# Kernel tuning notes

Measured on AMD Instinct MI355X. Metric: run time of the kernel, lower is better.

## Reference

```python
import jax, jax.numpy as jnp
import numpy as np

B, L, N, D = 4096, 50, 50, 128
STD = 0.1


def setup_inputs() -> dict:
    key = jax.random.key(0)
    ks = jax.random.split(key, 6)
    seq_idx = jax.random.randint(ks[0], (B, L), 0, N, dtype=jnp.int32)
    mask = jnp.ones((B, L), dtype=jnp.int32)
    node_vectors = jax.random.normal(ks[1], (B, N, D), dtype=jnp.float32)
    u = lambda k, shp: jax.random.uniform(k, shp, jnp.float32, -STD, STD)
    return {
        "sequence_of_indexes": seq_idx,
        "mask": mask,
        "node_vectors": node_vectors,
        "batch_size": B,
        "W_last": u(ks[2], (D, D)),      # dense_last_item kernel (no bias)
        "W_seq": u(ks[3], (D, D)),       # dense_sequence_items kernel
        "b_seq": jnp.zeros((D,), jnp.float32),  # dense_sequence_items bias
        "W_alpha": u(ks[4], (D, 1)),     # dense_alpha kernel (no bias)
    }


def reference(sequence_of_indexes, mask, node_vectors, batch_size,
              W_last, W_seq, b_seq, W_alpha):
    maskf = mask.astype(jnp.float32)                          # [B, L]
    seq_len = jnp.sum(maskf, axis=1).astype(jnp.int32)        # [B]
    rows = jnp.arange(batch_size)
    # last item index per session, then gather its node vector
    last_idx = sequence_of_indexes[rows, seq_len - 1]         # [B]
    v_n = node_vectors[rows, last_idx]                        # [B, D]
    # per-batch embedding lookup: node_vectors[b, seq_idx[b]]
    v_i = jnp.take_along_axis(node_vectors, sequence_of_indexes[..., None], axis=1)  # [B, L, D]
    vn_proj = (v_n @ W_last)[:, None, :]                      # [B, 1, D]
    vi_proj = v_i @ W_seq + b_seq                             # [B, L, D]
    alpha = jax.nn.sigmoid(vn_proj + vi_proj) @ W_alpha       # [B, L, 1]
    alpha = alpha * maskf[..., None]
    session_graph = jnp.sum(alpha * v_i, axis=1)              # [B, D]
    return v_n, session_graph
```

## Files before the change

kernel.cpp:

```cpp
#include <hip/hip_runtime.h>
#include <math.h>

#define BB 4096
#define LL 50
#define NN 50
#define DD 128
#define STR 136

typedef short bf16x8 __attribute__((ext_vector_type(8)));
typedef float f32x4  __attribute__((ext_vector_type(4)));

static __device__ inline unsigned short f32_to_bf16_rne(float f) {
    unsigned int u = __float_as_uint(f);
    u += 0x7FFFu + ((u >> 16) & 1u);
    return (unsigned short)(u >> 16);
}

__global__ void prep_w(const float* __restrict__ W_seq,
                       const float* __restrict__ W_last,
                       unsigned short* __restrict__ ws)
{
    int t = blockIdx.x * blockDim.x + threadIdx.x;
    int lane = t & 63;
    int nt   = (t >> 6) & 7;
    int kk   = t >> 9;
    const float* W = (kk < 4) ? W_seq : W_last;
    int kb = (kk & 3) * 32 + (lane >> 4) * 8;
    int n  = nt * 16 + (lane & 15);
    unsigned short* dst = ws + (size_t)t * 8;
    #pragma unroll
    for (int j = 0; j < 8; ++j)
        dst[j] = f32_to_bf16_rne(W[(kb + j) * DD + n]);
}

__global__ __launch_bounds__(256, 4) void sess_attn(
    const int*   __restrict__ seq_idx,
    const int*   __restrict__ mask,
    const float* __restrict__ nodes,
    const float* __restrict__ b_seq,
    const float* __restrict__ W_alpha,
    const unsigned short* __restrict__ wfrag,
    float*       __restrict__ out)
{
    const int b    = blockIdx.x;
    const int tid  = threadIdx.x;
    const int lane = tid & 63;
    const int wave = tid >> 6;
    const int col  = lane & 15;
    const int quad = lane >> 4;

    __shared__ __align__(16) float s_f[NN * DD];
    __shared__ __align__(16) unsigned short s_nbf[NN * STR];
    __shared__ float s_alpha[64];
    __shared__ float s_cnt[64];
    __shared__ int   s_last;

    const float* nb = nodes + (size_t)b * (NN * DD);

    int pm = 0, pi = 0;
    if (tid < 64) {
        pm = (tid < LL) ? mask[b * LL + tid]    : 0;
        pi = (tid < LL) ? seq_idx[b * LL + tid] : 0;
    }

    #pragma unroll
    for (int i = 0; i < 6; ++i) {
        int p  = i * 256 + tid;
        int r  = p >> 5;
        int Bk = p & 31;
        const float* src = nb + r * DD + ((Bk ^ (r & 7)) << 2);
        __builtin_amdgcn_global_load_lds(
            (const __attribute__((address_space(1))) unsigned int*)src,
            (__attribute__((address_space(3))) unsigned int*)(&s_f[(i * 256 + wave * 64) * 4]),
            16, 0, 0);
    }
    if (tid < 64) {
        int p  = 1536 + tid;
        int r  = p >> 5, Bk = p & 31;
        const float* src = nb + r * DD + ((Bk ^ (r & 7)) << 2);
        __builtin_amdgcn_global_load_lds(
            (const __attribute__((address_space(1))) unsigned int*)src,
            (__attribute__((address_space(3))) unsigned int*)(&s_f[1536 * 4]),
            16, 0, 0);
    }

    const bf16x8* wsf = (const bf16x8*)wfrag;
    bf16x8 bfS[8], bfL[8];
    #pragma unroll
    for (int kk = 0; kk < 4; ++kk)
        #pragma unroll
        for (int j2 = 0; j2 < 2; ++j2) {
            bfS[kk * 2 + j2] = wsf[(size_t)(((kk    ) * 8 + wave * 2 + j2) * 64 + lane)];
            bfL[kk * 2 + j2] = wsf[(size_t)(((kk + 4) * 8 + wave * 2 + j2) * 64 + lane)];
        }

    float bb_r[2], wa_r[2];
    #pragma unroll
    for (int j2 = 0; j2 < 2; ++j2) {
        int n = (wave * 2 + j2) * 16 + col;
        bb_r[j2] = b_seq[n];
        wa_r[j2] = W_alpha[n];
    }

    if (tid < 64) { s_alpha[tid] = 0.f; s_cnt[tid] = 0.f; }

    asm volatile("s_waitcnt vmcnt(0)" ::: "memory");
    #pragma unroll
    for (int i = 0; i < 6; ++i) {
        int p  = i * 256 + wave * 64 + lane;
        int r  = p >> 5, Bk = p & 31;
        float4 f = *(const float4*)&s_f[p * 4];
        ushort4 h;
        h.x = f32_to_bf16_rne(f.x);
        h.y = f32_to_bf16_rne(f.y);
        h.z = f32_to_bf16_rne(f.z);
        h.w = f32_to_bf16_rne(f.w);
        *(ushort4*)&s_nbf[r * STR + ((Bk ^ (r & 7)) << 2)] = h;
    }
    if (tid < 64) {
        int p  = 1536 + lane;
        int r  = p >> 5, Bk = p & 31;
        float4 f = *(const float4*)&s_f[p * 4];
        ushort4 h;
        h.x = f32_to_bf16_rne(f.x);
        h.y = f32_to_bf16_rne(f.y);
        h.z = f32_to_bf16_rne(f.z);
        h.w = f32_to_bf16_rne(f.w);
        *(ushort4*)&s_nbf[r * STR + ((Bk ^ (r & 7)) << 2)] = h;
    }

    if (tid < 64) {
        int mm = pm;
        mm += __shfl_xor(mm, 1);  mm += __shfl_xor(mm, 2);
        mm += __shfl_xor(mm, 4);  mm += __shfl_xor(mm, 8);
        mm += __shfl_xor(mm, 16); mm += __shfl_xor(mm, 32);
        int jl = mm - 1;
        if (jl < 0) jl += LL;
        int li = __shfl(pi, jl);
        if (tid == 0) s_last = li;
        if (tid < LL && pm) atomicAdd(&s_cnt[pi], (float)pm);
    }

    __syncthreads();

    const int last = s_last;
    const int sL   = last & 7;

    if (tid < DD)
        out[(size_t)b * DD + tid] =
            s_f[last * DD + (((tid >> 2) ^ sL) << 2) + (tid & 3)];

    f32x4 acc[4][2];
    #pragma unroll
    for (int m = 0; m < 4; ++m)
        #pragma unroll
        for (int j2 = 0; j2 < 2; ++j2)
            acc[m][j2] = (f32x4){0.f, 0.f, 0.f, 0.f};
    f32x4 accV[2];
    #pragma unroll
    for (int j2 = 0; j2 < 2; ++j2)
        accV[j2] = (f32x4){bb_r[j2], bb_r[j2], bb_r[j2], bb_r[j2]};

    #pragma unroll
    for (int kk = 0; kk < 4; ++kk) {
        const int co = kk * 32 + quad * 8;
        bf16x8 a[4];
        #pragma unroll
        for (int m = 0; m < 4; ++m) {
            int r = m * 16 + col;
            if (r > NN - 1) r = NN - 1;
            a[m] = *(const bf16x8*)&s_nbf[r * STR + co];
        }
        bf16x8 av = *(const bf16x8*)&s_nbf[last * STR + co];
        #pragma unroll
        for (int j2 = 0; j2 < 2; ++j2) {
            acc[0][j2] = __builtin_amdgcn_mfma_f32_16x16x32_bf16(a[0], bfS[kk * 2 + j2], acc[0][j2], 0, 0, 0);
            acc[1][j2] = __builtin_amdgcn_mfma_f32_16x16x32_bf16(a[1], bfS[kk * 2 + j2], acc[1][j2], 0, 0, 0);
            acc[2][j2] = __builtin_amdgcn_mfma_f32_16x16x32_bf16(a[2], bfS[kk * 2 + j2], acc[2][j2], 0, 0, 0);
            acc[3][j2] = __builtin_amdgcn_mfma_f32_16x16x32_bf16(a[3], bfS[kk * 2 + j2], acc[3][j2], 0, 0, 0);
            accV[j2]   = __builtin_amdgcn_mfma_f32_16x16x32_bf16(av,   bfL[kk * 2 + j2], accV[j2],   0, 0, 0);
        }
    }

    #pragma unroll
    for (int m = 0; m < 4; ++m) {
        float pr[4] = {0.f, 0.f, 0.f, 0.f};
        #pragma unroll
        for (int j2 = 0; j2 < 2; ++j2) {
            float waj = wa_r[j2];
            #pragma unroll
            for (int r = 0; r < 4; ++r) {
                float x = acc[m][j2][r] + accV[j2][r];
                float sig = 1.f / (1.f + __expf(-x));
                pr[r] = fmaf(sig, waj, pr[r]);
            }
        }
        #pragma unroll
        for (int r = 0; r < 4; ++r) {
            float vv = pr[r];
            vv += __shfl_xor(vv, 1);
            vv += __shfl_xor(vv, 2);
            vv += __shfl_xor(vv, 4);
            vv += __shfl_xor(vv, 8);
            int row = m * 16 + quad * 4 + r;
            if (col == 0 && row < NN) atomicAdd(&s_alpha[row], vv);
        }
    }
    __syncthreads();

    if (tid < DD) {
        const int Bd = tid >> 2, od = tid & 3;
        float acc2 = 0.f;
        #pragma unroll 10
        for (int n = 0; n < NN; ++n)
            acc2 = fmaf(s_cnt[n] * s_alpha[n],
                        s_f[n * DD + ((Bd ^ (n & 7)) << 2) + od], acc2);
        out[(size_t)BB * DD + (size_t)b * DD + tid] = acc2;
    }
}

extern "C" void kernel_launch(void* const* d_in, const int* in_sizes, int n_in,
                              void* d_out, int out_size, void* d_ws, size_t ws_size,
                              hipStream_t stream) {
    const int*   seq     = (const int*)  d_in[0];
    const int*   mask    = (const int*)  d_in[1];
    const float* nodes   = (const float*)d_in[2];
    const float* W_last  = (const float*)d_in[4];
    const float* W_seq   = (const float*)d_in[5];
    const float* b_seq   = (const float*)d_in[6];
    const float* W_alpha = (const float*)d_in[7];
    float*       out     = (float*)      d_out;

    unsigned short* wsf = (unsigned short*)d_ws;

    prep_w<<<16, 256, 0, stream>>>(W_seq, W_last, wsf);
    sess_attn<<<BB, 256, 0, stream>>>(seq, mask, nodes, b_seq, W_alpha, wsf, out);
}
```

Baseline: 179.2 us.

## Process eight sessions per block with double-buffered bf16 tiles and prefetch

Each block now handles eight consecutive batch entries. The next entry's node vectors are prefetched into LDS while the current one is multiplied, and the converted bf16 tile is double-buffered. Weight fragments and per-block setup are amortised over the eight entries, and the final weighted sum reads the bf16 tile instead of fp32. This reduces the grid to 512 blocks and lowers occupancy, risking poorer latency hiding, and slightly lowers the precision of the output sum.

```diff
diff --git a/kernel.cpp b/kernel.cpp
--- a/kernel.cpp
+++ b/kernel.cpp
@@ -6,14 +6,22 @@
 #define NN 50
 #define DD 128
 #define STR 136
+#define NB 8
+#define GRID 512
 
 typedef short bf16x8 __attribute__((ext_vector_type(8)));
 typedef float f32x4  __attribute__((ext_vector_type(4)));
+
+#define AS1 __attribute__((address_space(1)))
+#define AS3 __attribute__((address_space(3)))
 
 static __device__ inline unsigned short f32_to_bf16_rne(float f) {
     unsigned int u = __float_as_uint(f);
     u += 0x7FFFu + ((u >> 16) & 1u);
     return (unsigned short)(u >> 16);
+}
+static __device__ inline float bf16_to_f32(unsigned short h) {
+    return __uint_as_float(((unsigned int)h) << 16);
 }
 
 __global__ void prep_w(const float* __restrict__ W_seq,
@@ -33,7 +41,7 @@
         dst[j] = f32_to_bf16_rne(W[(kb + j) * DD + n]);
 }
 
-__global__ __launch_bounds__(256, 4) void sess_attn(
+__global__ __launch_bounds__(256, 2) void sess_attn(
     const int*   __restrict__ seq_idx,
     const int*   __restrict__ mask,
     const float* __restrict__ nodes,
@@ -42,46 +50,40 @@
     const unsigned short* __restrict__ wfrag,
     float*       __restrict__ out)
 {
-    const int b    = blockIdx.x;
+    const int blk  = blockIdx.x;
     const int tid  = threadIdx.x;
     const int lane = tid & 63;
     const int wave = tid >> 6;
     const int col  = lane & 15;
     const int quad = lane >> 4;
 
-    __shared__ __align__(16) float s_f[NN * DD];
-    __shared__ __align__(16) unsigned short s_nbf[NN * STR];
-    __shared__ float s_alpha[64];
-    __shared__ float s_cnt[64];
-    __shared__ int   s_last;
-
-    const float* nb = nodes + (size_t)b * (NN * DD);
-
-    int pm = 0, pi = 0;
-    if (tid < 64) {
-        pm = (tid < LL) ? mask[b * LL + tid]    : 0;
-        pi = (tid < LL) ? seq_idx[b * LL + tid] : 0;
-    }
-
-    #pragma unroll
-    for (int i = 0; i < 6; ++i) {
-        int p  = i * 256 + tid;
-        int r  = p >> 5;
-        int Bk = p & 31;
-        const float* src = nb + r * DD + ((Bk ^ (r & 7)) << 2);
-        __builtin_amdgcn_global_load_lds(
-            (const __attribute__((address_space(1))) unsigned int*)src,
-            (__attribute__((address_space(3))) unsigned int*)(&s_f[(i * 256 + wave * 64) * 4]),
-            16, 0, 0);
-    }
-    if (tid < 64) {
-        int p  = 1536 + tid;
-        int r  = p >> 5, Bk = p & 31;
-        const float* src = nb + r * DD + ((Bk ^ (r & 7)) << 2);
-        __builtin_amdgcn_global_load_lds(
-            (const __attribute__((address_space(1))) unsigned int*)src,
-            (__attribute__((address_space(3))) unsigned int*)(&s_f[1536 * 4]),
-            16, 0, 0);
+    __shared__ __align__(16) float          s_f[NN * DD];
+    __shared__ __align__(16) unsigned short s_nbf[2][NN * STR];
+    __shared__ float s_alpha[2][64];
+    __shared__ float s_cnt[NB][64];
+    __shared__ __align__(16) int s_mask[NB * LL];
+    __shared__ __align__(16) int s_sidx[NB * LL];
+    __shared__ int   s_last[NB];
+
+    const int b0 = blk * NB;
+
+    int4 m4, s4;
+    if (tid < 100) {
+        m4 = ((const int4*)(mask    + b0 * LL))[tid];
+        s4 = ((const int4*)(seq_idx + b0 * LL))[tid];
+    }
+
+    {
+        const float* nb = nodes + (size_t)b0 * (NN * DD);
+        #pragma unroll
+        for (int c = 0; c < 6; ++c)
+            __builtin_amdgcn_global_load_lds(
+                (const AS1 unsigned int*)(nb + (size_t)(c * 256 + tid) * 4),
+                (AS3 unsigned int*)(&s_f[(c * 256 + wave * 64) * 4]), 16, 0, 0);
+        if (tid < 64)
+            __builtin_amdgcn_global_load_lds(
+                (const AS1 unsigned int*)(nb + (size_t)(1536 + tid) * 4),
+                (AS3 unsigned int*)(&s_f[1536 * 4]), 16, 0, 0);
     }
 
     const bf16x8* wsf = (const bf16x8*)wfrag;
@@ -93,7 +95,6 @@
             bfS[kk * 2 + j2] = wsf[(size_t)(((kk    ) * 8 + wave * 2 + j2) * 64 + lane)];
             bfL[kk * 2 + j2] = wsf[(size_t)(((kk + 4) * 8 + wave * 2 + j2) * 64 + lane)];
         }
-
     float bb_r[2], wa_r[2];
     #pragma unroll
     for (int j2 = 0; j2 < 2; ++j2) {
@@ -102,34 +103,21 @@
         wa_r[j2] = W_alpha[n];
     }
 
-    if (tid < 64) { s_alpha[tid] = 0.f; s_cnt[tid] = 0.f; }
-
-    asm volatile("s_waitcnt vmcnt(0)" ::: "memory");
-    #pragma unroll
-    for (int i = 0; i < 6; ++i) {
-        int p  = i * 256 + wave * 64 + lane;
-        int r  = p >> 5, Bk = p & 31;
-        float4 f = *(const float4*)&s_f[p * 4];
-        ushort4 h;
-        h.x = f32_to_bf16_rne(f.x);
-        h.y = f32_to_bf16_rne(f.y);
-        h.z = f32_to_bf16_rne(f.z);
-        h.w = f32_to_bf16_rne(f.w);
-        *(ushort4*)&s_nbf[r * STR + ((Bk ^ (r & 7)) << 2)] = h;
-    }
-    if (tid < 64) {
-        int p  = 1536 + lane;
-        int r  = p >> 5, Bk = p & 31;
-        float4 f = *(const float4*)&s_f[p * 4];
-        ushort4 h;
-        h.x = f32_to_bf16_rne(f.x);
-        h.y = f32_to_bf16_rne(f.y);
-        h.z = f32_to_bf16_rne(f.z);
-        h.w = f32_to_bf16_rne(f.w);
-        *(ushort4*)&s_nbf[r * STR + ((Bk ^ (r & 7)) << 2)] = h;
-    }
-
-    if (tid < 64) {
+    #pragma unroll
+    for (int z = 0; z < 2; ++z) s_cnt[z * 4 + wave][lane] = 0.f;
+    if (tid < 64) { s_alpha[0][tid] = 0.f; s_alpha[1][tid] = 0.f; }
+    if (tid < 100) {
+        *(int4*)&s_mask[tid * 4] = m4;
+        *(int4*)&s_sidx[tid * 4] = s4;
+    }
+
+    __syncthreads();
+
+    #pragma unroll
+    for (int t2 = 0; t2 < 2; ++t2) {
+        int ib = wave * 2 + t2;
+        int pm = (lane < LL) ? s_mask[ib * LL + lane] : 0;
+        int pi = (lane < LL) ? s_sidx[ib * LL + lane] : 0;
         int mm = pm;
         mm += __shfl_xor(mm, 1);  mm += __shfl_xor(mm, 2);
         mm += __shfl_xor(mm, 4);  mm += __shfl_xor(mm, 8);
@@ -137,85 +125,130 @@
         int jl = mm - 1;
         if (jl < 0) jl += LL;
         int li = __shfl(pi, jl);
-        if (tid == 0) s_last = li;
-        if (tid < LL && pm) atomicAdd(&s_cnt[pi], (float)pm);
+        if (lane == 0) s_last[ib] = li;
+        if (lane < LL && pm) atomicAdd(&s_cnt[ib][pi], (float)pm);
     }
 
     __syncthreads();
 
-    const int last = s_last;
-    const int sL   = last & 7;
-
-    if (tid < DD)
-        out[(size_t)b * DD + tid] =
-            s_f[last * DD + (((tid >> 2) ^ sL) << 2) + (tid & 3)];
-
-    f32x4 acc[4][2];
-    #pragma unroll
-    for (int m = 0; m < 4; ++m)
+    const int r0 = col, r1 = 16 + col, r2 = 32 + col;
+    const int r3 = (48 + col > NN - 1) ? (NN - 1) : (48 + col);
+
+    for (int i = 0; i < NB; ++i) {
+        const int b   = b0 + i;
+        const int par = i & 1;
+
+        if (i >= 1 && tid < 64) s_alpha[(i - 1) & 1][tid] = 0.f;
+
+        #pragma unroll
+        for (int c = 0; c < 6; ++c) {
+            int p = c * 256 + tid;
+            int r = p >> 5, cc = (p & 31) * 4;
+            float4 f = *(const float4*)&s_f[p * 4];
+            ushort4 h;
+            h.x = f32_to_bf16_rne(f.x); h.y = f32_to_bf16_rne(f.y);
+            h.z = f32_to_bf16_rne(f.z); h.w = f32_to_bf16_rne(f.w);
+            *(ushort4*)&s_nbf[par][r * STR + cc] = h;
+        }
+        if (tid < 64) {
+            int p = 1536 + tid;
+            int r = p >> 5, cc = (p & 31) * 4;
+            float4 f = *(const float4*)&s_f[p * 4];
+            ushort4 h;
+            h.x = f32_to_bf16_rne(f.x); h.y = f32_to_bf16_rne(f.y);
+            h.z = f32_to_bf16_rne(f.z); h.w = f32_to_bf16_rne(f.w);
+            *(ushort4*)&s_nbf[par][r * STR + cc] = h;
+        }
+
+        __syncthreads();
+
+        if (i < NB - 1) {
+            const float* nb = nodes + (size_t)(b + 1) * (NN * DD);
+            #pragma unroll
+            for (int c = 0; c < 6; ++c)
+                __builtin_amdgcn_global_load_lds(
+                    (const AS1 unsigned int*)(nb + (size_t)(c * 256 + tid) * 4),
+                    (AS3 unsigned int*)(&s_f[(c * 256 + wave * 64) * 4]), 16, 0, 0);
+            if (tid < 64)
+                __builtin_amdgcn_global_load_lds(
+                    (const AS1 unsigned int*)(nb + (size_t)(1536 + tid) * 4),
+                    (AS3 unsigned int*)(&s_f[1536 * 4]), 16, 0, 0);
+        }
+
+        const int last = s_last[i];
+
+        if (tid < DD)
+            out[(size_t)b * DD + tid] =
+                nodes[(size_t)b * (NN * DD) + last * DD + tid];
+
+        f32x4 acc[4][2], accV[2];
+        #pragma unroll
+        for (int m = 0; m < 4; ++m)
+            #pragma unroll
+            for (int j2 = 0; j2 < 2; ++j2)
+                acc[m][j2] = (f32x4){0.f, 0.f, 0.f, 0.f};
         #pragma unroll
         for (int j2 = 0; j2 < 2; ++j2)
-            acc[m][j2] = (f32x4){0.f, 0.f, 0.f, 0.f};
-    f32x4 accV[2];
-    #pragma unroll
-    for (int j2 = 0; j2 < 2; ++j2)
-        accV[j2] = (f32x4){bb_r[j2], bb_r[j2], bb_r[j2], bb_r[j2]};
-
-    #pragma unroll
-    for (int kk = 0; kk < 4; ++kk) {
-        const int co = kk * 32 + quad * 8;
-        bf16x8 a[4];
+            accV[j2] = (f32x4){bb_r[j2], bb_r[j2], bb_r[j2], bb_r[j2]};
+
+        const unsigned short* tb = s_nbf[par];
+        #pragma unroll
+        for (int kk = 0; kk < 4; ++kk) {
+            const int co = kk * 32 + quad * 8;
+            bf16x8 a0 = *(const bf16x8*)&tb[r0 * STR + co];
+            bf16x8 a1 = *(const bf16x8*)&tb[r1 * STR + co];
+            bf16x8 a2 = *(const bf16x8*)&tb[r2 * STR + co];
+            bf16x8 a3 = *(const bf16x8*)&tb[r3 * STR + co];
+            bf16x8 av = *(const bf16x8*)&tb[last * STR + co];
+            #pragma unroll
+            for (int j2 = 0; j2 < 2; ++j2) {
+                acc[0][j2] = __builtin_amdgcn_mfma_f32_16x16x32_bf16(a0, bfS[kk * 2 + j2], acc[0][j2], 0, 0, 0);
+                acc[1][j2] = __builtin_amdgcn_mfma_f32_16x16x32_bf16(a1, bfS[kk * 2 + j2], acc[1][j2], 0, 0, 0);
+                acc[2][j2] = __builtin_amdgcn_mfma_f32_16x16x32_bf16(a2, bfS[kk * 2 + j2], acc[2][j2], 0, 0, 0);
+                acc[3][j2] = __builtin_amdgcn_mfma_f32_16x16x32_bf16(a3, bfS[kk * 2 + j2], acc[3][j2], 0, 0, 0);
+                accV[j2]   = __builtin_amdgcn_mfma_f32_16x16x32_bf16(av, bfL[kk * 2 + j2], accV[j2],   0, 0, 0);
+            }
+        }
+
         #pragma unroll
         for (int m = 0; m < 4; ++m) {
-            int r = m * 16 + col;
-            if (r > NN - 1) r = NN - 1;
-            a[m] = *(const bf16x8*)&s_nbf[r * STR + co];
-        }
-        bf16x8 av = *(const bf16x8*)&s_nbf[last * STR + co];
-        #pragma unroll
-        for (int j2 = 0; j2 < 2; ++j2) {
-            acc[0][j2] = __builtin_amdgcn_mfma_f32_16x16x32_bf16(a[0], bfS[kk * 2 + j2], acc[0][j2], 0, 0, 0);
-            acc[1][j2] = __builtin_amdgcn_mfma_f32_16x16x32_bf16(a[1], bfS[kk * 2 + j2], acc[1][j2], 0, 0, 0);
-            acc[2][j2] = __builtin_amdgcn_mfma_f32_16x16x32_bf16(a[2], bfS[kk * 2 + j2], acc[2][j2], 0, 0, 0);
-            acc[3][j2] = __builtin_amdgcn_mfma_f32_16x16x32_bf16(a[3], bfS[kk * 2 + j2], acc[3][j2], 0, 0, 0);
-            accV[j2]   = __builtin_amdgcn_mfma_f32_16x16x32_bf16(av,   bfL[kk * 2 + j2], accV[j2],   0, 0, 0);
-        }
-    }
-
-    #pragma unroll
-    for (int m = 0; m < 4; ++m) {
-        float pr[4] = {0.f, 0.f, 0.f, 0.f};
-        #pragma unroll
-        for (int j2 = 0; j2 < 2; ++j2) {
-            float waj = wa_r[j2];
+            float pr[4] = {0.f, 0.f, 0.f, 0.f};
+            #pragma unroll
+            for (int j2 = 0; j2 < 2; ++j2) {
+                float waj = wa_r[j2];
+                #pragma unroll
+                for (int r = 0; r < 4; ++r) {
+                    float x = acc[m][j2][r] + accV[j2][r];
+                    pr[r] = fmaf(1.f / (1.f + __expf(-x)), waj, pr[r]);
+                }
+            }
             #pragma unroll
             for (int r = 0; r < 4; ++r) {
-                float x = acc[m][j2][r] + accV[j2][r];
-                float sig = 1.f / (1.f + __expf(-x));
-                pr[r] = fmaf(sig, waj, pr[r]);
-            }
-        }
-        #pragma unroll
-        for (int r = 0; r < 4; ++r) {
-            float vv = pr[r];
-            vv += __shfl_xor(vv, 1);
-            vv += __shfl_xor(vv, 2);
-            vv += __shfl_xor(vv, 4);
-            vv += __shfl_xor(vv, 8);
-            int row = m * 16 + quad * 4 + r;
-            if (col == 0 && row < NN) atomicAdd(&s_alpha[row], vv);
-        }
-    }
-    __syncthreads();
-
-    if (tid < DD) {
-        const int Bd = tid >> 2, od = tid & 3;
-        float acc2 = 0.f;
-        #pragma unroll 10
-        for (int n = 0; n < NN; ++n)
-            acc2 = fmaf(s_cnt[n] * s_alpha[n],
-                        s_f[n * DD + ((Bd ^ (n & 7)) << 2) + od], acc2);
-        out[(size_t)BB * DD + (size_t)b * DD + tid] = acc2;
+                float vv = pr[r];
+                vv += __shfl_xor(vv, 1);
+                vv += __shfl_xor(vv, 2);
+                vv += __shfl_xor(vv, 4);
+                vv += __shfl_xor(vv, 8);
+                int row = m * 16 + quad * 4 + r;
+                if (col == 0 && row < NN) atomicAdd(&s_alpha[par][row], vv);
+            }
+        }
+
+        __syncthreads();
+
+        if (tid < DD) {
+            float accA = 0.f, accB = 0.f;
+            #pragma unroll 5
+            for (int n = 0; n < NN; n += 2) {
+                float wA = s_cnt[i][n]     * s_alpha[par][n];
+                float wB = s_cnt[i][n + 1] * s_alpha[par][n + 1];
+                accA = fmaf(wA, bf16_to_f32(tb[n * STR + tid]), accA);
+                accB = fmaf(wB, bf16_to_f32(tb[(n + 1) * STR + tid]), accB);
+            }
+            out[(size_t)BB * DD + (size_t)b * DD + tid] = accA + accB;
+        }
+
+        __syncthreads();
     }
 }
 
@@ -234,5 +267,5 @@
     unsigned short* wsf = (unsigned short*)d_ws;
 
     prep_w<<<16, 256, 0, stream>>>(W_seq, W_last, wsf);
-    sess_attn<<<BB, 256, 0, stream>>>(seq, mask, nodes, b_seq, W_alpha, wsf, out);
-}
+    sess_attn<<<GRID, 256, 0, stream>>>(seq, mask, nodes, b_seq, W_alpha, wsf, out);
+}
```

Result: slower. 194.3 us (+8.4%).
